# Kernel optimization log

Measured on AMD Instinct MI355X. Metric: run time of the kernel, lower is better.

Reference implementation:

```python
import jax, jax.numpy as jnp
import numpy as np

N_NODES = 100000


def gcn_conv(x, W, b, src, dst, n_nodes):
    # x: [N, Fin], W: [Fin, Fout], edge (src->dst) with self-loops added,
    # symmetric normalization D^{-1/2} A D^{-1/2} as in PyG GCNConv defaults.
    h = x @ W  # [N, Fout]
    loops = jnp.arange(n_nodes, dtype=src.dtype)
    src_all = jnp.concatenate([src, loops])
    dst_all = jnp.concatenate([dst, loops])
    ones = jnp.ones(src_all.shape[0], dtype=h.dtype)
    deg = jax.ops.segment_sum(ones, dst_all, num_segments=n_nodes)  # in-degree incl. self-loop
    dinv = jnp.where(deg > 0, jax.lax.rsqrt(deg), 0.0)
    norm = dinv[src_all] * dinv[dst_all]  # [E+N]
    msg = h[src_all] * norm[:, None]      # gather + scale
    out = jax.ops.segment_sum(msg, dst_all, num_segments=n_nodes)  # scatter-add
    return out + b


def setup_inputs() -> dict:
    key = jax.random.key(0)
    k1, k2, k3, k4 = jax.random.split(key, 4)
    in_dim, hidden, out_dim = 128, 128, 64
    n_edges = 600000
    x = jax.random.normal(k1, (N_NODES, in_dim), dtype=jnp.float32)
    edge_index = jax.random.randint(k2, (2, n_edges), 0, N_NODES, dtype=jnp.int64)
    # Glorot-ish init for weights
    W1 = jax.random.normal(k3, (in_dim, hidden), dtype=jnp.float32) / np.sqrt(in_dim)
    b1 = jnp.zeros((hidden,), dtype=jnp.float32)
    W2 = jax.random.normal(k4, (hidden, out_dim), dtype=jnp.float32) / np.sqrt(hidden)
    b2 = jnp.zeros((out_dim,), dtype=jnp.float32)
    return {"x": x, "edge_index": edge_index, "W1": W1, "b1": b1, "W2": W2, "b2": b2}


def reference(x, edge_index, W1, b1, W2, b2):
    src, dst = edge_index[0], edge_index[1]
    h = jax.nn.relu(gcn_conv(x, W1, b1, src, dst, N_NODES))
    # dropout is identity in eval mode (training=False)
    return gcn_conv(h, W2, b2, src, dst, N_NODES)
```

## Files before the change

kernel.cpp:

```cpp
#include <hip/hip_runtime.h>
#include <hip/hip_bf16.h>
#include <stdint.h>

typedef unsigned int u32;
typedef unsigned short u16;
typedef __attribute__((ext_vector_type(8))) short short8;
typedef __attribute__((ext_vector_type(4))) float f32x4;

#define SCAN_TILE 2048

__device__ __forceinline__ float bf2f(u16 u) {
    union { u32 u; float f; } v; v.u = ((u32)u) << 16; return v.f;
}
__device__ __forceinline__ u16 f2bf(float f) {
    u32 u = __float_as_uint(f);
    u32 r = (u + 0x7FFFu + ((u >> 16) & 1u)) >> 16;
    return (u16)r;
}
__device__ __forceinline__ u32 packbf(float lo, float hi) {
    return ((u32)f2bf(hi) << 16) | (u32)f2bf(lo);
}

__global__ __launch_bounds__(256) void detect_k(const u32* __restrict__ xw,
                                                const u32* __restrict__ ew,
                                                int* __restrict__ flags) {
    __shared__ int cnt;
    __shared__ u32 orr;
    int t = threadIdx.x;
    if (t == 0) { cnt = 0; orr = 0u; }
    __syncthreads();
    int hits = 0;
    for (int i = t; i < 1024; i += 256) {
        u32 f = (xw[i] >> 7) & 0xFFu;
        if (f >= 100u && f <= 140u) hits++;
    }
    atomicAdd(&cnt, hits);
    atomicOr(&orr, ew[2 * t + 1]);
    __syncthreads();
    if (t == 0) {
        flags[0] = (cnt < 512) ? 1 : 0;
        flags[1] = (orr == 0u) ? 1 : 0;
    }
}

template<int N>
__global__ __launch_bounds__(256) void w_pack_k(const void* __restrict__ W,
                                                uint4* __restrict__ wpk,
                                                const int* __restrict__ flags) {
    const int p = blockIdx.x * 256 + threadIdx.x;
    if (p >= 16 * N) return;
    const int n = p & (N - 1);
    const int kb = p >> ((N == 128) ? 7 : 6);
    u32 pk[4];
    if (flags[0]) {
        const float* wp = (const float*)W + (size_t)(kb * 8) * N + n;
        #pragma unroll
        for (int jj = 0; jj < 4; jj++)
            pk[jj] = packbf(wp[(2 * jj) * N], wp[(2 * jj + 1) * N]);
    } else {
        const u16* wp = (const u16*)W + (size_t)(kb * 8) * N + n;
        #pragma unroll
        for (int jj = 0; jj < 4; jj++)
            pk[jj] = ((u32)wp[(2 * jj + 1) * N] << 16) | (u32)wp[(2 * jj) * N];
    }
    uint4 v; v.x = pk[0]; v.y = pk[1]; v.z = pk[2]; v.w = pk[3];
    wpk[p] = v;
}

__global__ __launch_bounds__(256) void count_deg_k(const void* __restrict__ ei, int E,
                                                   const int* __restrict__ flags,
                                                   int* __restrict__ deg) {
    int i = blockIdx.x * 256 + threadIdx.x;
    if (i >= E) return;
    int d = flags[1] ? (int)((const long long*)ei)[E + i] : ((const int*)ei)[E + i];
    atomicAdd(&deg[d], 1);
}

__global__ __launch_bounds__(256) void scan_partial_k(const int* __restrict__ deg, int M,
                                                      int* __restrict__ bsum) {
    const int t = threadIdx.x;
    const int base = blockIdx.x * SCAN_TILE + t * 8;
    int s = 0;
    if (base + 8 <= M) {
        int4 a = *(const int4*)(deg + base);
        int4 b = *(const int4*)(deg + base + 4);
        s = a.x + a.y + a.z + a.w + b.x + b.y + b.z + b.w;
    } else {
        for (int j = 0; j < 8; j++) if (base + j < M) s += deg[base + j];
    }
    __shared__ int red[256];
    red[t] = s;
    __syncthreads();
    for (int d = 128; d > 0; d >>= 1) {
        if (t < d) red[t] += red[t + d];
        __syncthreads();
    }
    if (t == 0) bsum[blockIdx.x] = red[0];
}

__global__ __launch_bounds__(256) void scan_bsum_k(int* __restrict__ bsum, int nb,
                                                   int* __restrict__ off, int M) {
    __shared__ int buf[2][256];
    const int t = threadIdx.x;
    int v = (t < nb) ? bsum[t] : 0;
    const int own = v;
    buf[0][t] = v;
    __syncthreads();
    int cur = 0;
    for (int d = 1; d < 256; d <<= 1) {
        int x = buf[cur][t];
        if (t >= d) x += buf[cur][t - d];
        buf[cur ^ 1][t] = x;
        __syncthreads();
        cur ^= 1;
    }
    if (t < nb) bsum[t] = buf[cur][t] - own;
    if (t == 255) off[M] = buf[cur][255];
}

__global__ __launch_bounds__(256) void scan_final_k(const int* __restrict__ deg,
                                                    const int* __restrict__ bsum, int M,
                                                    int* __restrict__ off,
                                                    int* __restrict__ cursor,
                                                    float* __restrict__ dinv) {
    const int t = threadIdx.x;
    const int base = blockIdx.x * SCAN_TILE + t * 8;
    int v[8];
    int s = 0;
    const bool full = (base + 8 <= M);
    if (full) {
        int4 a = *(const int4*)(deg + base);
        int4 b = *(const int4*)(deg + base + 4);
        v[0] = a.x; v[1] = a.y; v[2] = a.z; v[3] = a.w;
        v[4] = b.x; v[5] = b.y; v[6] = b.z; v[7] = b.w;
        s = v[0] + v[1] + v[2] + v[3] + v[4] + v[5] + v[6] + v[7];
    } else {
        #pragma unroll
        for (int j = 0; j < 8; j++) { v[j] = (base + j < M) ? deg[base + j] : 0; s += v[j]; }
    }
    __shared__ int buf[2][256];
    buf[0][t] = s;
    __syncthreads();
    int cur = 0;
    for (int d = 1; d < 256; d <<= 1) {
        int x = buf[cur][t];
        if (t >= d) x += buf[cur][t - d];
        buf[cur ^ 1][t] = x;
        __syncthreads();
        cur ^= 1;
    }
    int pre = bsum[blockIdx.x] + buf[cur][t] - s;
    int o[8]; float dv[8];
    #pragma unroll
    for (int j = 0; j < 8; j++) {
        o[j] = pre;
        dv[j] = rsqrtf((float)(v[j] + 1));
        pre += v[j];
    }
    if (full) {
        *(int4*)(off + base)     = make_int4(o[0], o[1], o[2], o[3]);
        *(int4*)(off + base + 4) = make_int4(o[4], o[5], o[6], o[7]);
        *(int4*)(cursor + base)     = make_int4(o[0], o[1], o[2], o[3]);
        *(int4*)(cursor + base + 4) = make_int4(o[4], o[5], o[6], o[7]);
        *(float4*)(dinv + base)     = make_float4(dv[0], dv[1], dv[2], dv[3]);
        *(float4*)(dinv + base + 4) = make_float4(dv[4], dv[5], dv[6], dv[7]);
    } else {
        for (int j = 0; j < 8; j++) if (base + j < M) {
            off[base + j] = o[j]; cursor[base + j] = o[j]; dinv[base + j] = dv[j];
        }
    }
}

__global__ __launch_bounds__(256) void fill_k(const void* __restrict__ ei, int E,
                                              const int* __restrict__ flags,
                                              int* __restrict__ cursor, int* __restrict__ eidx) {
    int i = blockIdx.x * 256 + threadIdx.x;
    if (i >= E) return;
    int s, d;
    if (flags[1]) { const long long* p = (const long long*)ei; s = (int)p[i]; d = (int)p[E + i]; }
    else          { const int* p = (const int*)ei;             s = p[i];      d = p[E + i]; }
    int pos = atomicAdd(&cursor[d], 1);
    eidx[pos] = s;
}

template<int N>
__global__ __launch_bounds__(256) void gemm_mfma_k(
    const void* __restrict__ X, const uint4* __restrict__ wpk,
    const float* __restrict__ dinv, u16* __restrict__ HS,
    const int* __restrict__ flags, int x_is_ext, int M)
{
    constexpr int NT = N / 16;
    constexpr int NC8 = N / 8;
    __shared__ u32 xlds[128 * 64];
    const int t = threadIdx.x;
    const int wave = t >> 6, lane = t & 63;
    const int q = lane >> 4, m = lane & 15;
    const bool xf32 = (x_is_ext != 0) && (flags[0] != 0);
    const int row0 = blockIdx.x * 128;

    for (int c = t; c < 2048; c += 256) {
        const int row = c >> 4, c8 = c & 15;
        const int grow = row0 + row;
        uint4 pk = make_uint4(0u, 0u, 0u, 0u);
        if (grow < M) {
            if (xf32) {
                const float* xp = (const float*)X + (size_t)grow * 128 + c8 * 8;
                float4 u = *(const float4*)xp;
                float4 v = *(const float4*)(xp + 4);
                pk.x = packbf(u.x, u.y); pk.y = packbf(u.z, u.w);
                pk.z = packbf(v.x, v.y); pk.w = packbf(v.z, v.w);
            } else {
                pk = *(const uint4*)((const u16*)X + (size_t)grow * 128 + c8 * 8);
            }
        }
        *(uint4*)&xlds[row * 64 + c8 * 4] = pk;
    }
    __syncthreads();

    union { uint4 u; short8 v; } a[2][4];
    #pragma unroll
    for (int rt = 0; rt < 2; rt++)
        #pragma unroll
        for (int s = 0; s < 4; s++)
            a[rt][s].u = *(const uint4*)&xlds[(wave * 32 + rt * 16 + m) * 64 + (s * 4 + q) * 4];

    f32x4 acc[2][NT];
    #pragma unroll
    for (int rt = 0; rt < 2; rt++)
        #pragma unroll
        for (int tt = 0; tt < NT; tt++)
            acc[rt][tt] = (f32x4){0.f, 0.f, 0.f, 0.f};

    #pragma unroll
    for (int s = 0; s < 4; s++) {
        union { uint4 u; short8 v; } b[NT];
        #pragma unroll
        for (int tt = 0; tt < NT; tt++)
            b[tt].u = wpk[(s * 4 + q) * N + tt * 16 + m];
        #pragma unroll
        for (int tt = 0; tt < NT; tt++)
            #pragma unroll
            for (int rt = 0; rt < 2; rt++)
                acc[rt][tt] = __builtin_amdgcn_mfma_f32_16x16x32_bf16(
                    a[rt][s].v, b[tt].v, acc[rt][tt], 0, 0, 0);
    }

    float dv[2][4];
    #pragma unroll
    for (int rt = 0; rt < 2; rt++)
        #pragma unroll
        for (int r = 0; r < 4; r++) {
            const int grow = row0 + wave * 32 + rt * 16 + q * 4 + r;
            dv[rt][r] = (grow < M) ? dinv[grow] : 0.f;
        }

    u16* orow = (u16*)&xlds[wave * 32 * 64];
    #pragma unroll
    for (int rt = 0; rt < 2; rt++)
        #pragma unroll
        for (int tt = 0; tt < NT; tt++)
            #pragma unroll
            for (int r = 0; r < 4; r++)
                orow[(rt * 16 + q * 4 + r) * N + tt * 16 + m] =
                    f2bf(acc[rt][tt][r] * dv[rt][r]);

    constexpr int ITER = 16 * NC8 / 64;
    #pragma unroll
    for (int rt = 0; rt < 2; rt++) {
        #pragma unroll
        for (int j = 0; j < ITER; j++) {
            const int cc = lane + j * 64;
            const int lrow = cc / NC8, c8 = cc % NC8;
            const int grow = row0 + wave * 32 + rt * 16 + lrow;
            uint4 v = *(const uint4*)&((const u32*)orow)[(rt * 16 + lrow) * (N / 2) + c8 * 4];
            if (grow < M)
                *(uint4*)(HS + (size_t)grow * N + c8 * 8) = v;
        }
    }
}

template<int N, bool RELU>
__global__ __launch_bounds__(256) void aggregate_k(
    const u16* __restrict__ hs, const int* __restrict__ eidx,
    const int* __restrict__ off, const float* __restrict__ dinv,
    const void* __restrict__ bias, void* __restrict__ out,
    const int* __restrict__ flags, int out_is_ext, int M)
{
    constexpr int TPN = N / 8;
    constexpr int NPB = 256 / TPN;
    const int node = blockIdx.x * NPB + threadIdx.x / TPN;
    const int lane = threadIdx.x % TPN;
    if (node >= M) return;
    const int f32io = flags[0];
    const int beg = off[node], end = off[node + 1];
    const int c8 = lane * 8;
    const u16* __restrict__ hrow = hs + c8;

    float a[8];
    {
        uint4 sp = *(const uint4*)(hrow + (size_t)node * N);
        const u16* s = (const u16*)&sp;
        #pragma unroll
        for (int j = 0; j < 8; j++) a[j] = bf2f(s[j]);
    }

    int p = beg;
    for (; p + 4 <= end; p += 4) {
        const int s0 = eidx[p + 0], s1 = eidx[p + 1];
        const int s2 = eidx[p + 2], s3 = eidx[p + 3];
        uint4 v0 = *(const uint4*)(hrow + (size_t)s0 * N);
        uint4 v1 = *(const uint4*)(hrow + (size_t)s1 * N);
        uint4 v2 = *(const uint4*)(hrow + (size_t)s2 * N);
        uint4 v3 = *(const uint4*)(hrow + (size_t)s3 * N);
        const u16* q0 = (const u16*)&v0; const u16* q1 = (const u16*)&v1;
        const u16* q2 = (const u16*)&v2; const u16* q3 = (const u16*)&v3;
        #pragma unroll
        for (int j = 0; j < 8; j++)
            a[j] += (bf2f(q0[j]) + bf2f(q1[j])) + (bf2f(q2[j]) + bf2f(q3[j]));
    }
    for (; p < end; p++) {
        const int s = eidx[p];
        uint4 v = *(const uint4*)(hrow + (size_t)s * N);
        const u16* q = (const u16*)&v;
        #pragma unroll
        for (int j = 0; j < 8; j++) a[j] += bf2f(q[j]);
    }

    const float dv = dinv[node];
    float b[8];
    if (f32io) {
        float4 u = *(const float4*)((const float*)bias + c8);
        float4 v = *(const float4*)((const float*)bias + c8 + 4);
        b[0] = u.x; b[1] = u.y; b[2] = u.z; b[3] = u.w;
        b[4] = v.x; b[5] = v.y; b[6] = v.z; b[7] = v.w;
    } else {
        uint4 u = *(const uint4*)((const u16*)bias + c8);
        const u16* s = (const u16*)&u;
        #pragma unroll
        for (int j = 0; j < 8; j++) b[j] = bf2f(s[j]);
    }
    float o[8];
    #pragma unroll
    for (int j = 0; j < 8; j++) {
        o[j] = fmaf(dv, a[j], b[j]);
        if (RELU) o[j] = fmaxf(o[j], 0.f);
    }
    if (out_is_ext && f32io) {
        float* op = (float*)out + (size_t)node * N + c8;
        *(float4*)op       = make_float4(o[0], o[1], o[2], o[3]);
        *(float4*)(op + 4) = make_float4(o[4], o[5], o[6], o[7]);
    } else {
        uint4 pk;
        pk.x = packbf(o[0], o[1]); pk.y = packbf(o[2], o[3]);
        pk.z = packbf(o[4], o[5]); pk.w = packbf(o[6], o[7]);
        *(uint4*)((u16*)out + (size_t)node * N + c8) = pk;
    }
}

extern "C" void kernel_launch(void* const* d_in, const int* in_sizes, int n_in,
                              void* d_out, int out_size, void* d_ws, size_t ws_size,
                              hipStream_t stream) {
    const void* x  = d_in[0];
    const void* ei = d_in[1];
    const void* W1 = d_in[2];
    const void* b1 = d_in[3];
    const void* W2 = d_in[4];
    const void* b2 = d_in[5];

    const int M = in_sizes[0] / 128;
    const int E = in_sizes[1] / 2;
    const int NB = (M + SCAN_TILE - 1) / SCAN_TILE;

    char* ws = (char*)d_ws;
    size_t offb = 0;
    auto alloc = [&](size_t bytes) -> void* {
        void* p = ws + offb; offb += (bytes + 255) & ~(size_t)255; return p;
    };
    int*   flags  = (int*)  alloc(256);
    int*   bsum   = (int*)  alloc(1024);
    uint4* wpk1   = (uint4*)alloc(16 * 128 * 16);
    uint4* wpk2   = (uint4*)alloc(16 * 64 * 16);
    int*   deg    = (int*)  alloc((size_t)M * 4);
    int*   off    = (int*)  alloc((size_t)(M + 1) * 4);
    int*   cursor = (int*)  alloc((size_t)M * 4);
    float* dinv   = (float*)alloc((size_t)M * 4);
    int*   eidx   = (int*)  alloc((size_t)E * 4);
    u16*   hs1    = (u16*)  alloc((size_t)M * 128 * 2);
    u16*   out1   = (u16*)  alloc((size_t)M * 128 * 2);
    u16*   hs2    = hs1;
    (void)ws_size; (void)n_in; (void)out_size;

    detect_k<<<1, 256, 0, stream>>>((const u32*)x, (const u32*)ei, flags);
    w_pack_k<128><<<8, 256, 0, stream>>>(W1, wpk1, flags);
    w_pack_k<64><<<4, 256, 0, stream>>>(W2, wpk2, flags);

    hipMemsetAsync(deg, 0, (size_t)M * 4, stream);
    count_deg_k<<<(E + 255) / 256, 256, 0, stream>>>(ei, E, flags, deg);
    scan_partial_k<<<NB, 256, 0, stream>>>(deg, M, bsum);
    scan_bsum_k<<<1, 256, 0, stream>>>(bsum, NB, off, M);
    scan_final_k<<<NB, 256, 0, stream>>>(deg, bsum, M, off, cursor, dinv);
    fill_k<<<(E + 255) / 256, 256, 0, stream>>>(ei, E, flags, cursor, eidx);

    gemm_mfma_k<128><<<(M + 127) / 128, 256, 0, stream>>>(x, wpk1, dinv, hs1, flags, 1, M);
    aggregate_k<128, true><<<(M + 15) / 16, 256, 0, stream>>>(hs1, eidx, off, dinv, b1, out1,
                                                              flags, 0, M);
    gemm_mfma_k<64><<<(M + 127) / 128, 256, 0, stream>>>(out1, wpk2, dinv, hs2, flags, 0, M);
    aggregate_k<64, false><<<(M + 31) / 32, 256, 0, stream>>>(hs2, eidx, off, dinv, b2, d_out,
                                                              flags, 1, M);
}
```

Baseline: 248.3 us.

## Merge setup kernels, vectorize edge loads, halve GEMM tile rows

Folds the degree memset into the format-detection kernel and merges the two weight-packing launches into one, cutting launch count. The degree-count and CSR-fill kernels now have each thread handle two edges through vector loads. The MFMA GEMM drops from 128 to 64 rows per block, giving more blocks and lower LDS use per block. The second hidden buffer gets its own allocation instead of aliasing hs1, which takes more workspace.

```diff
diff --git a/kernel.cpp b/kernel.cpp
--- a/kernel.cpp
+++ b/kernel.cpp
@@ -21,38 +21,41 @@
     return ((u32)f2bf(hi) << 16) | (u32)f2bf(lo);
 }
 
-__global__ __launch_bounds__(256) void detect_k(const u32* __restrict__ xw,
-                                                const u32* __restrict__ ew,
-                                                int* __restrict__ flags) {
-    __shared__ int cnt;
-    __shared__ u32 orr;
-    int t = threadIdx.x;
-    if (t == 0) { cnt = 0; orr = 0u; }
-    __syncthreads();
-    int hits = 0;
-    for (int i = t; i < 1024; i += 256) {
-        u32 f = (xw[i] >> 7) & 0xFFu;
-        if (f >= 100u && f <= 140u) hits++;
-    }
-    atomicAdd(&cnt, hits);
-    atomicOr(&orr, ew[2 * t + 1]);
-    __syncthreads();
-    if (t == 0) {
-        flags[0] = (cnt < 512) ? 1 : 0;
-        flags[1] = (orr == 0u) ? 1 : 0;
+__global__ __launch_bounds__(256) void detect_zero_k(const u32* __restrict__ xw,
+                                                     const u32* __restrict__ ew,
+                                                     int* __restrict__ flags,
+                                                     int* __restrict__ deg, int M) {
+    const int t = threadIdx.x;
+    const int i4 = (blockIdx.x * 256 + t) * 4;
+    if (i4 + 4 <= M) *(int4*)(deg + i4) = make_int4(0, 0, 0, 0);
+    else { for (int j = 0; j < 4; j++) if (i4 + j < M) deg[i4 + j] = 0; }
+
+    if (blockIdx.x == 0) {
+        __shared__ int cnt;
+        __shared__ u32 orr;
+        if (t == 0) { cnt = 0; orr = 0u; }
+        __syncthreads();
+        int hits = 0;
+        for (int i = t; i < 1024; i += 256) {
+            u32 f = (xw[i] >> 7) & 0xFFu;
+            if (f >= 100u && f <= 140u) hits++;
+        }
+        atomicAdd(&cnt, hits);
+        atomicOr(&orr, ew[2 * t + 1]);
+        __syncthreads();
+        if (t == 0) {
+            flags[0] = (cnt < 512) ? 1 : 0;
+            flags[1] = (orr == 0u) ? 1 : 0;
+        }
     }
 }
 
 template<int N>
-__global__ __launch_bounds__(256) void w_pack_k(const void* __restrict__ W,
-                                                uint4* __restrict__ wpk,
-                                                const int* __restrict__ flags) {
-    const int p = blockIdx.x * 256 + threadIdx.x;
-    if (p >= 16 * N) return;
+__device__ __forceinline__ void wpack_one(const void* W, uint4* wpk, int p, int f32w) {
     const int n = p & (N - 1);
     const int kb = p >> ((N == 128) ? 7 : 6);
     u32 pk[4];
-    if (flags[0]) {
+    if (f32w) {
         const float* wp = (const float*)W + (size_t)(kb * 8) * N + n;
         #pragma unroll
         for (int jj = 0; jj < 4; jj++)
@@ -65,15 +68,39 @@
     }
     uint4 v; v.x = pk[0]; v.y = pk[1]; v.z = pk[2]; v.w = pk[3];
     wpk[p] = v;
+}
+
+__global__ __launch_bounds__(256) void wpack_all_k(const void* __restrict__ W1,
+                                                   const void* __restrict__ W2,
+                                                   uint4* __restrict__ wpk1,
+                                                   uint4* __restrict__ wpk2,
+                                                   const int* __restrict__ flags) {
+    const int b = blockIdx.x, t = threadIdx.x;
+    const int f32w = flags[0];
+    if (b < 8) wpack_one<128>(W1, wpk1, b * 256 + t, f32w);
+    else       wpack_one<64> (W2, wpk2, (b - 8) * 256 + t, f32w);
 }
 
 __global__ __launch_bounds__(256) void count_deg_k(const void* __restrict__ ei, int E,
                                                    const int* __restrict__ flags,
                                                    int* __restrict__ deg) {
-    int i = blockIdx.x * 256 + threadIdx.x;
-    if (i >= E) return;
-    int d = flags[1] ? (int)((const long long*)ei)[E + i] : ((const int*)ei)[E + i];
-    atomicAdd(&deg[d], 1);
+    const int i2 = (blockIdx.x * 256 + threadIdx.x) * 2;
+    if (i2 >= E) return;
+    if (flags[1]) {
+        const long long* dp = (const long long*)ei + E;
+        if (i2 + 1 < E) {
+            longlong2 v = *(const longlong2*)(dp + i2);
+            atomicAdd(&deg[(int)v.x], 1);
+            atomicAdd(&deg[(int)v.y], 1);
+        } else atomicAdd(&deg[(int)dp[i2]], 1);
+    } else {
+        const int* dp = (const int*)ei + E;
+        if (i2 + 1 < E) {
+            int2 v = *(const int2*)(dp + i2);
+            atomicAdd(&deg[v.x], 1);
+            atomicAdd(&deg[v.y], 1);
+        } else atomicAdd(&deg[dp[i2]], 1);
+    }
 }
 
 __global__ __launch_bounds__(256) void scan_partial_k(const int* __restrict__ deg, int M,
@@ -174,13 +201,34 @@
 __global__ __launch_bounds__(256) void fill_k(const void* __restrict__ ei, int E,
                                               const int* __restrict__ flags,
                                               int* __restrict__ cursor, int* __restrict__ eidx) {
-    int i = blockIdx.x * 256 + threadIdx.x;
-    if (i >= E) return;
-    int s, d;
-    if (flags[1]) { const long long* p = (const long long*)ei; s = (int)p[i]; d = (int)p[E + i]; }
-    else          { const int* p = (const int*)ei;             s = p[i];      d = p[E + i]; }
-    int pos = atomicAdd(&cursor[d], 1);
-    eidx[pos] = s;
+    const int i2 = (blockIdx.x * 256 + threadIdx.x) * 2;
+    if (i2 >= E) return;
+    int s0, d0, s1 = -1, d1 = -1;
+    if (flags[1]) {
+        const long long* sp = (const long long*)ei;
+        const long long* dp = sp + E;
+        if (i2 + 1 < E) {
+            longlong2 sv = *(const longlong2*)(sp + i2);
+            longlong2 dv = *(const longlong2*)(dp + i2);
+            s0 = (int)sv.x; s1 = (int)sv.y; d0 = (int)dv.x; d1 = (int)dv.y;
+        } else { s0 = (int)sp[i2]; d0 = (int)dp[i2]; }
+    } else {
+        const int* sp = (const int*)ei;
+        const int* dp = sp + E;
+        if (i2 + 1 < E) {
+            int2 sv = *(const int2*)(sp + i2);
+            int2 dv = *(const int2*)(dp + i2);
+            s0 = sv.x; s1 = sv.y; d0 = dv.x; d1 = dv.y;
+        } else { s0 = sp[i2]; d0 = dp[i2]; }
+    }
+    int p0 = atomicAdd(&cursor[d0], 1);
+    eidx[p0] = s0;
+    if (s1 >= 0 || d1 >= 0) {
+        if (i2 + 1 < E) {
+            int p1 = atomicAdd(&cursor[d1], 1);
+            eidx[p1] = s1;
+        }
+    }
 }
 
 template<int N>
@@ -191,14 +239,14 @@
 {
     constexpr int NT = N / 16;
     constexpr int NC8 = N / 8;
-    __shared__ u32 xlds[128 * 64];
+    __shared__ u32 xlds[64 * 64];
     const int t = threadIdx.x;
     const int wave = t >> 6, lane = t & 63;
     const int q = lane >> 4, m = lane & 15;
     const bool xf32 = (x_is_ext != 0) && (flags[0] != 0);
-    const int row0 = blockIdx.x * 128;
-
-    for (int c = t; c < 2048; c += 256) {
+    const int row0 = blockIdx.x * 64;
+
+    for (int c = t; c < 1024; c += 256) {
         const int row = c >> 4, c8 = c & 15;
         const int grow = row0 + row;
         uint4 pk = make_uint4(0u, 0u, 0u, 0u);
@@ -217,19 +265,15 @@
     }
     __syncthreads();
 
-    union { uint4 u; short8 v; } a[2][4];
-    #pragma unroll
-    for (int rt = 0; rt < 2; rt++)
-        #pragma unroll
-        for (int s = 0; s < 4; s++)
-            a[rt][s].u = *(const uint4*)&xlds[(wave * 32 + rt * 16 + m) * 64 + (s * 4 + q) * 4];
-
-    f32x4 acc[2][NT];
-    #pragma unroll
-    for (int rt = 0; rt < 2; rt++)
-        #pragma unroll
-        for (int tt = 0; tt < NT; tt++)
-            acc[rt][tt] = (f32x4){0.f, 0.f, 0.f, 0.f};
+    union { uint4 u; short8 v; } a[4];
+    #pragma unroll
+    for (int s = 0; s < 4; s++)
+        a[s].u = *(const uint4*)&xlds[(wave * 16 + m) * 64 + (s * 4 + q) * 4];
+
+    f32x4 acc[NT];
+    #pragma unroll
+    for (int tt = 0; tt < NT; tt++)
+        acc[tt] = (f32x4){0.f, 0.f, 0.f, 0.f};
 
     #pragma unroll
     for (int s = 0; s < 4; s++) {
@@ -239,43 +283,33 @@
             b[tt].u = wpk[(s * 4 + q) * N + tt * 16 + m];
         #pragma unroll
         for (int tt = 0; tt < NT; tt++)
-            #pragma unroll
-            for (int rt = 0; rt < 2; rt++)
-                acc[rt][tt] = __builtin_amdgcn_mfma_f32_16x16x32_bf16(
-                    a[rt][s].v, b[tt].v, acc[rt][tt], 0, 0, 0);
-    }
-
-    float dv[2][4];
-    #pragma unroll
-    for (int rt = 0; rt < 2; rt++)
-        #pragma unroll
-        for (int r = 0; r < 4; r++) {
-            const int grow = row0 + wave * 32 + rt * 16 + q * 4 + r;
-            dv[rt][r] = (grow < M) ? dinv[grow] : 0.f;
-        }
-
-    u16* orow = (u16*)&xlds[wave * 32 * 64];
-    #pragma unroll
-    for (int rt = 0; rt < 2; rt++)
-        #pragma unroll
-        for (int tt = 0; tt < NT; tt++)
-            #pragma unroll
-            for (int r = 0; r < 4; r++)
-                orow[(rt * 16 + q * 4 + r) * N + tt * 16 + m] =
-                    f2bf(acc[rt][tt][r] * dv[rt][r]);
+            acc[tt] = __builtin_amdgcn_mfma_f32_16x16x32_bf16(
+                a[s].v, b[tt].v, acc[tt], 0, 0, 0);
+    }
+
+    float dv[4];
+    #pragma unroll
+    for (int r = 0; r < 4; r++) {
+        const int grow = row0 + wave * 16 + q * 4 + r;
+        dv[r] = (grow < M) ? dinv[grow] : 0.f;
+    }
+
+    u16* orow = (u16*)&xlds[wave * 16 * 64];
+    #pragma unroll
+    for (int tt = 0; tt < NT; tt++)
+        #pragma unroll
+        for (int r = 0; r < 4; r++)
+            orow[(q * 4 + r) * N + tt * 16 + m] = f2bf(acc[tt][r] * dv[r]);
 
     constexpr int ITER = 16 * NC8 / 64;
     #pragma unroll
-    for (int rt = 0; rt < 2; rt++) {
-        #pragma unroll
-        for (int j = 0; j < ITER; j++) {
-            const int cc = lane + j * 64;
-            const int lrow = cc / NC8, c8 = cc % NC8;
-            const int grow = row0 + wave * 32 + rt * 16 + lrow;
-            uint4 v = *(const uint4*)&((const u32*)orow)[(rt * 16 + lrow) * (N / 2) + c8 * 4];
-            if (grow < M)
-                *(uint4*)(HS + (size_t)grow * N + c8 * 8) = v;
-        }
+    for (int j = 0; j < ITER; j++) {
+        const int cc = lane + j * 64;
+        const int lrow = cc / NC8, c8 = cc % NC8;
+        const int grow = row0 + wave * 16 + lrow;
+        uint4 v = *(const uint4*)&((const u32*)orow)[lrow * (N / 2) + c8 * 4];
+        if (grow < M)
+            *(uint4*)(HS + (size_t)grow * N + c8 * 8) = v;
     }
 }
 
@@ -387,24 +421,22 @@
     int*   eidx   = (int*)  alloc((size_t)E * 4);
     u16*   hs1    = (u16*)  alloc((size_t)M * 128 * 2);
     u16*   out1   = (u16*)  alloc((size_t)M * 128 * 2);
-    u16*   hs2    = hs1;
+    u16*   hs2    = (u16*)  alloc((size_t)M * 64 * 2);
     (void)ws_size; (void)n_in; (void)out_size;
 
-    detect_k<<<1, 256, 0, stream>>>((const u32*)x, (const u32*)ei, flags);
-    w_pack_k<128><<<8, 256, 0, stream>>>(W1, wpk1, flags);
-    w_pack_k<64><<<4, 256, 0, stream>>>(W2, wpk2, flags);
-
-    hipMemsetAsync(deg, 0, (size_t)M * 4, stream);
-    count_deg_k<<<(E + 255) / 256, 256, 0, stream>>>(ei, E, flags, deg);
+    detect_zero_k<<<(M + 1023) / 1024, 256, 0, stream>>>((const u32*)x, (const u32*)ei,
+                                                         flags, deg, M);
+    wpack_all_k<<<12, 256, 0, stream>>>(W1, W2, wpk1, wpk2, flags);
+    count_deg_k<<<(E + 511) / 512, 256, 0, stream>>>(ei, E, flags, deg);
     scan_partial_k<<<NB, 256, 0, stream>>>(deg, M, bsum);
     scan_bsum_k<<<1, 256, 0, stream>>>(bsum, NB, off, M);
     scan_final_k<<<NB, 256, 0, stream>>>(deg, bsum, M, off, cursor, dinv);
-    fill_k<<<(E + 255) / 256, 256, 0, stream>>>(ei, E, flags, cursor, eidx);
-
-    gemm_mfma_k<128><<<(M + 127) / 128, 256, 0, stream>>>(x, wpk1, dinv, hs1, flags, 1, M);
+    fill_k<<<(E + 511) / 512, 256, 0, stream>>>(ei, E, flags, cursor, eidx);
+
+    gemm_mfma_k<128><<<(M + 63) / 64, 256, 0, stream>>>(x, wpk1, dinv, hs1, flags, 1, M);
     aggregate_k<128, true><<<(M + 15) / 16, 256, 0, stream>>>(hs1, eidx, off, dinv, b1, out1,
                                                               flags, 0, M);
-    gemm_mfma_k<64><<<(M + 127) / 128, 256, 0, stream>>>(out1, wpk2, dinv, hs2, flags, 0, M);
+    gemm_mfma_k<64><<<(M + 63) / 64, 256, 0, stream>>>(out1, wpk2, dinv, hs2, flags, 0, M);
     aggregate_k<64, false><<<(M + 31) / 32, 256, 0, stream>>>(hs2, eidx, off, dinv, b2, d_out,
                                                               flags, 1, M);
 }
```

Result: faster. 243.1 us (-2.1%).
